# Performance work log

Measured on AMD Instinct MI355X. Metric: run time of the kernel, lower is better.

Reference implementation:

```python
import jax, jax.numpy as jnp
from jax import lax
import numpy as np


def setup_inputs() -> dict:
    key = jax.random.key(0)
    ks = jax.random.split(key, 9)
    B, T, H, HALF, TGT = 512, 256, 512, 256, 28
    s = 1.0 / np.sqrt(H)  # torch LSTMCell/Linear default uniform scale (approx)
    return {
        "sequence": jax.random.normal(ks[0], (B, T, 1), jnp.float32),
        "W_ih": jax.random.normal(ks[1], (4 * H, 1), jnp.float32) * s,
        "W_hh": jax.random.normal(ks[2], (4 * H, H), jnp.float32) * s,
        "b_ih": jax.random.normal(ks[3], (4 * H,), jnp.float32) * s,
        "b_hh": jax.random.normal(ks[4], (4 * H,), jnp.float32) * s,
        "fc1_w": jax.random.normal(ks[5], (HALF, H), jnp.float32) * s,
        "fc1_b": jax.random.normal(ks[6], (HALF,), jnp.float32) * s,
        "fc2_w": jax.random.normal(ks[7], (TGT, HALF), jnp.float32) * (1.0 / np.sqrt(HALF)),
        "fc2_b": jax.random.normal(ks[8], (TGT,), jnp.float32) * (1.0 / np.sqrt(HALF)),
    }


def reference(sequence, W_ih, W_hh, b_ih, b_hh, fc1_w, fc1_b, fc2_w, fc2_b):
    B, T, _ = sequence.shape
    H = W_hh.shape[1]
    bias = b_ih + b_hh  # fuse the two bias adds

    def step(carry, x_t):
        h, c = carry
        # gates: [B, 4H]; PyTorch LSTMCell gate order is (i, f, g, o)
        gates = x_t @ W_ih.T + h @ W_hh.T + bias
        i, f, g, o = jnp.split(gates, 4, axis=-1)
        c = jax.nn.sigmoid(f) * c + jax.nn.sigmoid(i) * jnp.tanh(g)
        h = jax.nn.sigmoid(o) * jnp.tanh(c)
        return (h, c), None

    h0 = jnp.zeros((B, H), sequence.dtype)
    xs = jnp.swapaxes(sequence, 0, 1)  # [T, B, 1]
    (h, _), _ = lax.scan(step, (h0, h0), xs)

    hid = jax.nn.relu(h @ fc1_w.T + fc1_b)
    out = hid @ fc2_w.T + fc2_b  # [B, target_size]
    return out[:, :, None]  # [B, target_size, 1]
```

## Files before the change

### kernel.cpp

```cpp
#include <hip/hip_runtime.h>
#include <hip/hip_bf16.h>
#include <math.h>

#define BB   512
#define TT   256
#define HH   512
#define NCOL 2048
#define HALF 256
#define TGT  28

typedef short short8 __attribute__((ext_vector_type(8)));
typedef float f32x4  __attribute__((ext_vector_type(4)));

__device__ __forceinline__ float bf2f(unsigned short u) {
    union { unsigned int i; float f; } v; v.i = ((unsigned int)u) << 16; return v.f;
}
__device__ __forceinline__ unsigned short f2bf(float x) {
    union { float f; unsigned int i; } v; v.f = x;
    unsigned int u = v.i;
    return (unsigned short)((u + 0x7FFFu + ((u >> 16) & 1u)) >> 16);
}
__device__ __forceinline__ float sigmoidf_(float x) {
    return 1.0f / (1.0f + __expf(-x));
}
__device__ __forceinline__ float tanhf_(float x) {
    x = fminf(fmaxf(x, -15.0f), 15.0f);
    float e = __expf(-2.0f * x);
    return (1.0f - e) / (1.0f + e);
}

__device__ __forceinline__ int frag_addr(int r, int k) {
    return (r >> 4) * 8192 + (k >> 5) * 512 + ((((k >> 3) & 3) << 4) + (r & 15)) * 8 + (k & 7);
}

__device__ __forceinline__ void async_ld16(
    const unsigned short* gp, unsigned short* lp_base)
{
    __builtin_amdgcn_global_load_lds(
        (const __attribute__((address_space(1))) unsigned int*)gp,
        (__attribute__((address_space(3))) unsigned int*)lp_base,
        16, 0, 0x11);
}

__global__ __launch_bounds__(256) void prep_kernel(
    const float* __restrict__ Whh, const float* __restrict__ seq,
    unsigned short* __restrict__ Whi, unsigned short* __restrict__ Wlo,
    unsigned short* __restrict__ h0hi, unsigned short* __restrict__ h0lo,
    float* __restrict__ seqT, int* __restrict__ flags)
{
    int tid = blockIdx.x * 256 + threadIdx.x;
    h0hi[tid] = 0; h0lo[tid] = 0;
    if (tid < 16 * TT * 16) flags[tid] = 0;
    if (tid < BB * TT) {
        int b = tid >> 8, t = tid & (TT - 1);
        seqT[t * BB + b] = seq[tid];
    }
    for (int e = tid; e < NCOL * HH; e += 262144) {
        int n = e >> 9;
        int k = e & (HH - 1);
        int j = n >> 2, g = n & 3;
        float w = Whh[(g * HH + j) * HH + k];
        unsigned short hi = f2bf(w);
        float lo = w - bf2f(hi);
        int a = frag_addr(n, k);
        Whi[a] = hi;
        Wlo[a] = f2bf(lo);
    }
}

__global__ __launch_bounds__(512, 2) void lstm_persist(
    const unsigned short* __restrict__ Whi, const unsigned short* __restrict__ Wlo,
    unsigned short* __restrict__ h0hi, unsigned short* __restrict__ h0lo,
    unsigned short* __restrict__ h1hi, unsigned short* __restrict__ h1lo,
    const float* __restrict__ seqT,
    const float* __restrict__ wih,
    const float* __restrict__ bih, const float* __restrict__ bhh,
    int* __restrict__ flags)
{
    const int bid  = blockIdx.x;
    const int rg   = bid & 15;
    const int cb   = bid >> 4;
    const int tid  = threadIdx.x;
    const int lane = tid & 63;
    const int wave = tid >> 6;
    const int wn   = wave & 3, wk = wave >> 2;
    const int col16 = lane & 15, quad = lane >> 4;

    __shared__ __align__(16) short aS[32768];
    __shared__ __align__(16) float gS[2][32][132];

    short8 Wh[2][8], Wl[2][8];
    #pragma unroll
    for (int nt = 0; nt < 2; ++nt) {
        const int tb = (cb * 8 + wn * 2 + nt) * 8192 + lane * 8;
        #pragma unroll
        for (int kc = 0; kc < 8; ++kc) {
            const int a = tb + (wk * 8 + kc) * 512;
            Wh[nt][kc] = *(const short8*)(Whi + a);
            Wl[nt][kc] = *(const short8*)(Wlo + a);
        }
    }
    #pragma unroll
    for (int nt = 0; nt < 2; ++nt)
        #pragma unroll
        for (int kc = 0; kc < 8; ++kc) {
            asm volatile("" : "+v"(Wh[nt][kc]));
            asm volatile("" : "+v"(Wl[nt][kc]));
        }

    float bn[2], wxn[2];
    #pragma unroll
    for (int nt = 0; nt < 2; ++nt) {
        int n   = cb * 128 + wn * 32 + nt * 16 + col16;
        int src = (n & 3) * HH + (n >> 2);
        bn[nt]  = bih[src] + bhh[src];
        wxn[nt] = wih[src];
    }

    float creg[2] = {0.0f, 0.0f};

    int* myflags = flags + rg * (TT * 16);

    const int bb = tid >> 4;
    const int lj = (tid & 15) * 2;
    const int hbase = frag_addr(rg * 32 + bb, cb * 32 + lj);

    for (int t = 0; t < TT; ++t) {
        const unsigned short* hphi = (t & 1) ? h1hi : h0hi;
        const unsigned short* hplo = (t & 1) ? h1lo : h0lo;
        unsigned short* hnhi = (t & 1) ? h0hi : h1hi;
        unsigned short* hnlo = (t & 1) ? h0lo : h1lo;
        const unsigned short* hp_pl[2] = {hphi, hplo};

        float xr[2][4];
        if (wk == 0) {
            #pragma unroll
            for (int mt = 0; mt < 2; ++mt)
                #pragma unroll
                for (int r = 0; r < 4; ++r)
                    xr[mt][r] = seqT[t * BB + rg * 32 + mt * 16 + quad * 4 + r];
        }

        if (t > 0 && wave == 0) {
            const int* fp = myflags + (t - 1) * 16;
            long spins = 0;
            for (;;) {
                int f = 1;
                if (lane < 16)
                    f = __hip_atomic_load(fp + lane, __ATOMIC_RELAXED,
                                          __HIP_MEMORY_SCOPE_AGENT);
                if (__all(f != 0)) break;
                __builtin_amdgcn_s_sleep(1);
                if (++spins > 50000000L) break;
            }
        }
        __syncthreads();

        #pragma unroll
        for (int i = 0; i < 8; ++i) {
            const int j     = wave * 8 + i;
            const int plane = j >> 5;
            const int s     = (j & 31) * 512 + lane * 8;
            const int mt    = s >> 13;
            const unsigned short* gp =
                hp_pl[plane] + (rg * 2 + mt) * 8192 + (s & 8191);
            unsigned short* lp = (unsigned short*)aS + plane * 16384 + (j & 31) * 512;
            async_ld16(gp, lp);
        }
        __syncthreads();

        f32x4 acc[2][2];
        #pragma unroll
        for (int mt = 0; mt < 2; ++mt)
            #pragma unroll
            for (int nt = 0; nt < 2; ++nt)
                #pragma unroll
                for (int r = 0; r < 4; ++r)
                    acc[mt][nt][r] = (wk == 0)
                        ? bn[nt] + xr[mt][r] * wxn[nt] : 0.0f;

        const int abase = wk * 8 * 512 + lane * 8;
        #pragma unroll
        for (int kc = 0; kc < 8; ++kc) {
            const int o = abase + kc * 512;
            short8 ah0 = *(const short8*)((unsigned short*)aS + o);
            short8 ah1 = *(const short8*)((unsigned short*)aS + 8192 + o);
            short8 al0 = *(const short8*)((unsigned short*)aS + 16384 + o);
            short8 al1 = *(const short8*)((unsigned short*)aS + 16384 + 8192 + o);
            acc[0][0] = __builtin_amdgcn_mfma_f32_16x16x32_bf16(ah0, Wh[0][kc], acc[0][0], 0, 0, 0);
            acc[0][1] = __builtin_amdgcn_mfma_f32_16x16x32_bf16(ah0, Wh[1][kc], acc[0][1], 0, 0, 0);
            acc[1][0] = __builtin_amdgcn_mfma_f32_16x16x32_bf16(ah1, Wh[0][kc], acc[1][0], 0, 0, 0);
            acc[1][1] = __builtin_amdgcn_mfma_f32_16x16x32_bf16(ah1, Wh[1][kc], acc[1][1], 0, 0, 0);
            acc[0][0] = __builtin_amdgcn_mfma_f32_16x16x32_bf16(ah0, Wl[0][kc], acc[0][0], 0, 0, 0);
            acc[0][1] = __builtin_amdgcn_mfma_f32_16x16x32_bf16(ah0, Wl[1][kc], acc[0][1], 0, 0, 0);
            acc[1][0] = __builtin_amdgcn_mfma_f32_16x16x32_bf16(ah1, Wl[0][kc], acc[1][0], 0, 0, 0);
            acc[1][1] = __builtin_amdgcn_mfma_f32_16x16x32_bf16(ah1, Wl[1][kc], acc[1][1], 0, 0, 0);
            acc[0][0] = __builtin_amdgcn_mfma_f32_16x16x32_bf16(al0, Wh[0][kc], acc[0][0], 0, 0, 0);
            acc[0][1] = __builtin_amdgcn_mfma_f32_16x16x32_bf16(al0, Wh[1][kc], acc[0][1], 0, 0, 0);
            acc[1][0] = __builtin_amdgcn_mfma_f32_16x16x32_bf16(al1, Wh[0][kc], acc[1][0], 0, 0, 0);
            acc[1][1] = __builtin_amdgcn_mfma_f32_16x16x32_bf16(al1, Wh[1][kc], acc[1][1], 0, 0, 0);
        }

        #pragma unroll
        for (int mt = 0; mt < 2; ++mt)
            #pragma unroll
            for (int nt = 0; nt < 2; ++nt)
                #pragma unroll
                for (int r = 0; r < 4; ++r)
                    gS[wk][mt * 16 + quad * 4 + r][wn * 32 + nt * 16 + col16] = acc[mt][nt][r];
        __syncthreads();

        {
            f32x4 a0 = *(const f32x4*)(&gS[0][bb][lj * 4]);
            f32x4 b0 = *(const f32x4*)(&gS[1][bb][lj * 4]);
            f32x4 a1 = *(const f32x4*)(&gS[0][bb][(lj + 1) * 4]);
            f32x4 b1 = *(const f32x4*)(&gS[1][bb][(lj + 1) * 4]);
            float h_[2];
            #pragma unroll
            for (int e = 0; e < 2; ++e) {
                f32x4 ga = e ? a1 : a0, gb = e ? b1 : b0;
                float i_ = sigmoidf_(ga[0] + gb[0]);
                float f_ = sigmoidf_(ga[1] + gb[1]);
                float g_ = tanhf_(ga[2] + gb[2]);
                float o_ = sigmoidf_(ga[3] + gb[3]);
                float cn = f_ * creg[e] + i_ * g_;
                creg[e] = cn;
                h_[e] = o_ * tanhf_(cn);
            }
            unsigned short hh0 = f2bf(h_[0]), hh1 = f2bf(h_[1]);
            unsigned int hipk = (unsigned int)hh0 | ((unsigned int)hh1 << 16);
            unsigned int lopk = (unsigned int)f2bf(h_[0] - bf2f(hh0))
                              | ((unsigned int)f2bf(h_[1] - bf2f(hh1)) << 16);
            __hip_atomic_store((unsigned int*)(hnhi + hbase), hipk,
                               __ATOMIC_RELAXED, __HIP_MEMORY_SCOPE_AGENT);
            __hip_atomic_store((unsigned int*)(hnlo + hbase), lopk,
                               __ATOMIC_RELAXED, __HIP_MEMORY_SCOPE_AGENT);
        }

        __syncthreads();
        if (tid == 0)
            __hip_atomic_store(myflags + t * 16 + cb, 1, __ATOMIC_RELAXED,
                               __HIP_MEMORY_SCOPE_AGENT);
    }
}

__global__ __launch_bounds__(256) void fc_kernel(
    const unsigned short* __restrict__ hhi, const unsigned short* __restrict__ hlo,
    const float* __restrict__ fc1w, const float* __restrict__ fc1b,
    const float* __restrict__ fc2w, const float* __restrict__ fc2b,
    float* __restrict__ out)
{
    __shared__ float hS[HH];
    __shared__ float hidS[HALF];
    const int b = blockIdx.x, tid = threadIdx.x;

    for (int k = tid; k < HH; k += 256) {
        int a = frag_addr(b, k);
        hS[k] = bf2f(hhi[a]) + bf2f(hlo[a]);
    }
    __syncthreads();

    float acc = fc1b[tid];
    const float4* wrow = (const float4*)(fc1w + tid * HH);
    #pragma unroll 4
    for (int k4 = 0; k4 < HH / 4; ++k4) {
        float4 w = wrow[k4];
        acc += w.x * hS[k4 * 4] + w.y * hS[k4 * 4 + 1]
             + w.z * hS[k4 * 4 + 2] + w.w * hS[k4 * 4 + 3];
    }
    hidS[tid] = fmaxf(acc, 0.0f);
    __syncthreads();

    if (tid < TGT) {
        float a2 = fc2b[tid];
        const float4* w2 = (const float4*)(fc2w + tid * HALF);
        #pragma unroll 4
        for (int k4 = 0; k4 < HALF / 4; ++k4) {
            float4 w = w2[k4];
            a2 += w.x * hidS[k4 * 4] + w.y * hidS[k4 * 4 + 1]
                + w.z * hidS[k4 * 4 + 2] + w.w * hidS[k4 * 4 + 3];
        }
        out[b * TGT + tid] = a2;
    }
}

extern "C" void kernel_launch(void* const* d_in, const int* in_sizes, int n_in,
                              void* d_out, int out_size, void* d_ws, size_t ws_size,
                              hipStream_t stream)
{
    const float* seq   = (const float*)d_in[0];
    const float* W_ih  = (const float*)d_in[1];
    const float* W_hh  = (const float*)d_in[2];
    const float* b_ih  = (const float*)d_in[3];
    const float* b_hh  = (const float*)d_in[4];
    const float* fc1_w = (const float*)d_in[5];
    const float* fc1_b = (const float*)d_in[6];
    const float* fc2_w = (const float*)d_in[7];
    const float* fc2_b = (const float*)d_in[8];
    float* out = (float*)d_out;

    unsigned short* us = (unsigned short*)d_ws;
    unsigned short* Whi  = us;
    unsigned short* Wlo  = us + 1048576;
    unsigned short* h0hi = us + 2097152;
    unsigned short* h0lo = us + 2359296;
    unsigned short* h1hi = us + 2621440;
    unsigned short* h1lo = us + 2883584;
    float* seqT  = (float*)(us + 3145728);
    int*   flags = (int*)(seqT + BB * TT);

    prep_kernel<<<dim3(1024), dim3(256), 0, stream>>>(
        W_hh, seq, Whi, Wlo, h0hi, h0lo, seqT, flags);

    lstm_persist<<<dim3(256), dim3(512), 0, stream>>>(
        Whi, Wlo, h0hi, h0lo, h1hi, h1lo,
        seqT, W_ih, b_ih, b_hh, flags);

    fc_kernel<<<dim3(512), dim3(256), 0, stream>>>(
        h0hi, h0lo, fc1_w, fc1_b, fc2_w, fc2_b, out);
}
```

Baseline: 1.213 ms.

## Halve persistent LSTM block to 256 threads with four N-tiles per wave

```diff
diff --git a/kernel.cpp b/kernel.cpp
--- a/kernel.cpp
+++ b/kernel.cpp
@@ -68,7 +68,7 @@
     }
 }
 
-__global__ __launch_bounds__(512, 2) void lstm_persist(
+__global__ __launch_bounds__(256, 1) void lstm_persist(
     const unsigned short* __restrict__ Whi, const unsigned short* __restrict__ Wlo,
     unsigned short* __restrict__ h0hi, unsigned short* __restrict__ h0lo,
     unsigned short* __restrict__ h1hi, unsigned short* __restrict__ h1lo,
@@ -83,16 +83,17 @@
     const int tid  = threadIdx.x;
     const int lane = tid & 63;
     const int wave = tid >> 6;
-    const int wn   = wave & 3, wk = wave >> 2;
+    const int wn   = wave & 1;
+    const int wk   = wave >> 1;
     const int col16 = lane & 15, quad = lane >> 4;
 
     __shared__ __align__(16) short aS[32768];
-    __shared__ __align__(16) float gS[2][32][132];
-
-    short8 Wh[2][8], Wl[2][8];
+    __shared__ __align__(16) float gS[2][32][128];
+
+    short8 Wh[4][8], Wl[4][8];
     #pragma unroll
-    for (int nt = 0; nt < 2; ++nt) {
-        const int tb = (cb * 8 + wn * 2 + nt) * 8192 + lane * 8;
+    for (int nt = 0; nt < 4; ++nt) {
+        const int tb = (cb * 8 + wn * 4 + nt) * 8192 + lane * 8;
         #pragma unroll
         for (int kc = 0; kc < 8; ++kc) {
             const int a = tb + (wk * 8 + kc) * 512;
@@ -101,29 +102,34 @@
         }
     }
     #pragma unroll
-    for (int nt = 0; nt < 2; ++nt)
+    for (int nt = 0; nt < 4; ++nt)
         #pragma unroll
         for (int kc = 0; kc < 8; ++kc) {
             asm volatile("" : "+v"(Wh[nt][kc]));
             asm volatile("" : "+v"(Wl[nt][kc]));
         }
 
-    float bn[2], wxn[2];
+    float bn[4], wxn[4];
     #pragma unroll
-    for (int nt = 0; nt < 2; ++nt) {
-        int n   = cb * 128 + wn * 32 + nt * 16 + col16;
+    for (int nt = 0; nt < 4; ++nt) {
+        int n   = cb * 128 + wn * 64 + nt * 16 + col16;
         int src = (n & 3) * HH + (n >> 2);
         bn[nt]  = bih[src] + bhh[src];
         wxn[nt] = wih[src];
     }
 
-    float creg[2] = {0.0f, 0.0f};
+    float creg[4] = {0.0f, 0.0f, 0.0f, 0.0f};
 
     int* myflags = flags + rg * (TT * 16);
 
-    const int bb = tid >> 4;
-    const int lj = (tid & 15) * 2;
-    const int hbase = frag_addr(rg * 32 + bb, cb * 32 + lj);
+    int hbase[2], bbv[2], ljv[2];
+    #pragma unroll
+    for (int pp = 0; pp < 2; ++pp) {
+        int idx = tid + pp * 256;
+        bbv[pp] = idx >> 4;
+        ljv[pp] = (idx & 15) * 2;
+        hbase[pp] = frag_addr(rg * 32 + bbv[pp], cb * 32 + ljv[pp]);
+    }
 
     for (int t = 0; t < TT; ++t) {
         const unsigned short* hphi = (t & 1) ? h1hi : h0hi;
@@ -157,8 +163,8 @@
         __syncthreads();
 
         #pragma unroll
-        for (int i = 0; i < 8; ++i) {
-            const int j     = wave * 8 + i;
+        for (int i = 0; i < 16; ++i) {
+            const int j     = wave * 16 + i;
             const int plane = j >> 5;
             const int s     = (j & 31) * 512 + lane * 8;
             const int mt    = s >> 13;
@@ -169,48 +175,47 @@
         }
         __syncthreads();
 
-        f32x4 acc[2][2];
+        f32x4 acc[2][4];
         #pragma unroll
         for (int mt = 0; mt < 2; ++mt)
             #pragma unroll
-            for (int nt = 0; nt < 2; ++nt)
+            for (int nt = 0; nt < 4; ++nt)
                 #pragma unroll
                 for (int r = 0; r < 4; ++r)
                     acc[mt][nt][r] = (wk == 0)
                         ? bn[nt] + xr[mt][r] * wxn[nt] : 0.0f;
 
-        const int abase = wk * 8 * 512 + lane * 8;
+        const int abase = wk * 4096 + lane * 8;
         #pragma unroll
         for (int kc = 0; kc < 8; ++kc) {
             const int o = abase + kc * 512;
             short8 ah0 = *(const short8*)((unsigned short*)aS + o);
             short8 ah1 = *(const short8*)((unsigned short*)aS + 8192 + o);
             short8 al0 = *(const short8*)((unsigned short*)aS + 16384 + o);
-            short8 al1 = *(const short8*)((unsigned short*)aS + 16384 + 8192 + o);
-            acc[0][0] = __builtin_amdgcn_mfma_f32_16x16x32_bf16(ah0, Wh[0][kc], acc[0][0], 0, 0, 0);
-            acc[0][1] = __builtin_amdgcn_mfma_f32_16x16x32_bf16(ah0, Wh[1][kc], acc[0][1], 0, 0, 0);
-            acc[1][0] = __builtin_amdgcn_mfma_f32_16x16x32_bf16(ah1, Wh[0][kc], acc[1][0], 0, 0, 0);
-            acc[1][1] = __builtin_amdgcn_mfma_f32_16x16x32_bf16(ah1, Wh[1][kc], acc[1][1], 0, 0, 0);
-            acc[0][0] = __builtin_amdgcn_mfma_f32_16x16x32_bf16(ah0, Wl[0][kc], acc[0][0], 0, 0, 0);
-            acc[0][1] = __builtin_amdgcn_mfma_f32_16x16x32_bf16(ah0, Wl[1][kc], acc[0][1], 0, 0, 0);
-            acc[1][0] = __builtin_amdgcn_mfma_f32_16x16x32_bf16(ah1, Wl[0][kc], acc[1][0], 0, 0, 0);
-            acc[1][1] = __builtin_amdgcn_mfma_f32_16x16x32_bf16(ah1, Wl[1][kc], acc[1][1], 0, 0, 0);
-            acc[0][0] = __builtin_amdgcn_mfma_f32_16x16x32_bf16(al0, Wh[0][kc], acc[0][0], 0, 0, 0);
-            acc[0][1] = __builtin_amdgcn_mfma_f32_16x16x32_bf16(al0, Wh[1][kc], acc[0][1], 0, 0, 0);
-            acc[1][0] = __builtin_amdgcn_mfma_f32_16x16x32_bf16(al1, Wh[0][kc], acc[1][0], 0, 0, 0);
-            acc[1][1] = __builtin_amdgcn_mfma_f32_16x16x32_bf16(al1, Wh[1][kc], acc[1][1], 0, 0, 0);
+            short8 al1 = *(const short8*)((unsigned short*)aS + 24576 + o);
+            #pragma unroll
+            for (int nt = 0; nt < 4; ++nt) {
+                acc[0][nt] = __builtin_amdgcn_mfma_f32_16x16x32_bf16(ah0, Wh[nt][kc], acc[0][nt], 0, 0, 0);
+                acc[1][nt] = __builtin_amdgcn_mfma_f32_16x16x32_bf16(ah1, Wh[nt][kc], acc[1][nt], 0, 0, 0);
+                acc[0][nt] = __builtin_amdgcn_mfma_f32_16x16x32_bf16(ah0, Wl[nt][kc], acc[0][nt], 0, 0, 0);
+                acc[1][nt] = __builtin_amdgcn_mfma_f32_16x16x32_bf16(ah1, Wl[nt][kc], acc[1][nt], 0, 0, 0);
+                acc[0][nt] = __builtin_amdgcn_mfma_f32_16x16x32_bf16(al0, Wh[nt][kc], acc[0][nt], 0, 0, 0);
+                acc[1][nt] = __builtin_amdgcn_mfma_f32_16x16x32_bf16(al1, Wh[nt][kc], acc[1][nt], 0, 0, 0);
+            }
         }
 
         #pragma unroll
         for (int mt = 0; mt < 2; ++mt)
             #pragma unroll
-            for (int nt = 0; nt < 2; ++nt)
+            for (int nt = 0; nt < 4; ++nt)
                 #pragma unroll
                 for (int r = 0; r < 4; ++r)
-                    gS[wk][mt * 16 + quad * 4 + r][wn * 32 + nt * 16 + col16] = acc[mt][nt][r];
+                    gS[wk][mt * 16 + quad * 4 + r][wn * 64 + nt * 16 + col16] = acc[mt][nt][r];
         __syncthreads();
 
-        {
+        #pragma unroll
+        for (int pp = 0; pp < 2; ++pp) {
+            const int bb = bbv[pp], lj = ljv[pp];
             f32x4 a0 = *(const f32x4*)(&gS[0][bb][lj * 4]);
             f32x4 b0 = *(const f32x4*)(&gS[1][bb][lj * 4]);
             f32x4 a1 = *(const f32x4*)(&gS[0][bb][(lj + 1) * 4]);
@@ -223,17 +228,17 @@
                 float f_ = sigmoidf_(ga[1] + gb[1]);
                 float g_ = tanhf_(ga[2] + gb[2]);
                 float o_ = sigmoidf_(ga[3] + gb[3]);
-                float cn = f_ * creg[e] + i_ * g_;
-                creg[e] = cn;
+                float cn = f_ * creg[pp * 2 + e] + i_ * g_;
+                creg[pp * 2 + e] = cn;
                 h_[e] = o_ * tanhf_(cn);
             }
             unsigned short hh0 = f2bf(h_[0]), hh1 = f2bf(h_[1]);
             unsigned int hipk = (unsigned int)hh0 | ((unsigned int)hh1 << 16);
             unsigned int lopk = (unsigned int)f2bf(h_[0] - bf2f(hh0))
                               | ((unsigned int)f2bf(h_[1] - bf2f(hh1)) << 16);
-            __hip_atomic_store((unsigned int*)(hnhi + hbase), hipk,
+            __hip_atomic_store((unsigned int*)(hnhi + hbase[pp]), hipk,
                                __ATOMIC_RELAXED, __HIP_MEMORY_SCOPE_AGENT);
-            __hip_atomic_store((unsigned int*)(hnlo + hbase), lopk,
+            __hip_atomic_store((unsigned int*)(hnlo + hbase[pp]), lopk,
                                __ATOMIC_RELAXED, __HIP_MEMORY_SCOPE_AGENT);
         }
 
@@ -312,7 +317,7 @@
     prep_kernel<<<dim3(1024), dim3(256), 0, stream>>>(
         W_hh, seq, Whi, Wlo, h0hi, h0lo, seqT, flags);
 
-    lstm_persist<<<dim3(256), dim3(512), 0, stream>>>(
+    lstm_persist<<<dim3(256), dim3(256), 0, stream>>>(
         Whi, Wlo, h0hi, h0lo, h1hi, h1lo,
         seqT, W_ih, b_ih, b_hh, flags);
 
```

Measured after the change: 1.419 ms. 17.0% more time.
